# Kernel tuning notes

Hardware: AMD Instinct MI355X
Metric: run time of the kernel (lower is better)

Reference implementation:

```python
import jax, jax.numpy as jnp
import numpy as np

D_MODEL = 2048
N_LATENTS = 64
D_LATENT = 1024
N_HEADS = 16
D_H = D_LATENT // N_HEADS


def _split_heads(t):
    B, T, _ = t.shape
    return t.reshape(B, T, N_HEADS, D_H).transpose(0, 2, 1, 3)  # [B,H,T,d_h]


def _merge_heads(t):
    B, H, T, d = t.shape
    return t.transpose(0, 2, 1, 3).reshape(B, T, H * d)


def _attn(Q, K, V):
    scores = jnp.einsum('bhqd,bhkd->bhqk', Q, K) / jnp.sqrt(jnp.asarray(D_H, Q.dtype))
    w = jax.nn.softmax(scores, axis=-1)
    return jnp.einsum('bhqk,bhkd->bhqd', w, V)


def setup_inputs() -> dict:
    key = jax.random.key(0)
    ks = jax.random.split(key, 9)
    s_in = 1.0 / np.sqrt(D_MODEL)
    s_lat = 1.0 / np.sqrt(D_LATENT)
    return {
        'x': jax.random.normal(ks[0], (4, 4096, D_MODEL), dtype=jnp.float32),
        'L': jax.random.normal(ks[1], (N_LATENTS, D_LATENT), dtype=jnp.float32),
        'W_q_lat': jax.random.normal(ks[2], (D_LATENT, D_LATENT), dtype=jnp.float32) * s_lat,
        'W_k_in': jax.random.normal(ks[3], (D_MODEL, D_LATENT), dtype=jnp.float32) * s_in,
        'W_v_in': jax.random.normal(ks[4], (D_MODEL, D_LATENT), dtype=jnp.float32) * s_in,
        'W_q_in': jax.random.normal(ks[5], (D_MODEL, D_LATENT), dtype=jnp.float32) * s_in,
        'W_k_lat': jax.random.normal(ks[6], (D_LATENT, D_LATENT), dtype=jnp.float32) * s_lat,
        'W_v_lat': jax.random.normal(ks[7], (D_LATENT, D_LATENT), dtype=jnp.float32) * s_lat,
        'W_out': jax.random.normal(ks[8], (D_LATENT, D_MODEL), dtype=jnp.float32) * s_lat,
    }


def reference(x, L, W_q_lat, W_k_in, W_v_in, W_q_in, W_k_lat, W_v_lat, W_out):
    B = x.shape[0]
    Lb = jnp.broadcast_to(L[None], (B, N_LATENTS, D_LATENT))
    # Stage 1: latents attend to input tokens (cross-attention)
    Q = _split_heads(Lb @ W_q_lat)
    K = _split_heads(x @ W_k_in)
    V = _split_heads(x @ W_v_in)
    z = _merge_heads(_attn(Q, K, V))  # [B, n_latents, d_latent]
    # Stage 2: latent self-attention
    Ql = _split_heads(z @ W_q_lat)
    Kl = _split_heads(z @ W_k_lat)
    Vl = _split_heads(z @ W_v_lat)
    z2 = _merge_heads(_attn(Ql, Kl, Vl))
    # Stage 3: input tokens attend to latents (cross-attention back)
    Qx = _split_heads(x @ W_q_in)
    Kz = _split_heads(z2 @ W_k_lat)
    Vz = _split_heads(z2 @ W_v_lat)
    x_latent = _merge_heads(_attn(Qx, Kz, Vz))  # [B, N, d_latent]
    return x_latent @ W_out
```

## Files before the change

kernel.cpp:

```cpp
#include <hip/hip_runtime.h>


#define SEQ      4096
#define NHEADS   16
#define SCALE    0.125f

typedef short bfrag __attribute__((ext_vector_type(8)));
typedef float facc  __attribute__((ext_vector_type(4)));

__device__ __forceinline__ unsigned short f2bf(float f) {
  unsigned u = __float_as_uint(f);
  u += 0x7FFFu + ((u >> 16) & 1u);
  return (unsigned short)(u >> 16);
}
__device__ __forceinline__ float bf2f(unsigned short h) {
  return __uint_as_float(((unsigned)h) << 16);
}
__device__ __forceinline__ unsigned pack_hl(float a, float b, unsigned &lo) {
  unsigned short ha = f2bf(a), hb = f2bf(b);
  unsigned short la = f2bf(a - bf2f(ha)), lb = f2bf(b - bf2f(hb));
  lo = (unsigned)la | ((unsigned)lb << 16);
  return (unsigned)ha | ((unsigned)hb << 16);
}

__device__ __forceinline__ void gl_lds16(const void* g, void* l) {
  __builtin_amdgcn_global_load_lds(
      (const __attribute__((address_space(1))) void*)g,
      (__attribute__((address_space(3))) void*)l, 16, 0, 0);
}

__device__ __forceinline__ void write_split16(unsigned short* Hp, unsigned short* Lp,
                                              const float* o, float inv) {
  uint4 H0, H1, L0, L1;
  unsigned* Hw = &H0.x; unsigned* Lw = &L0.x;
#pragma unroll
  for (int k = 0; k < 8; k++) {
    unsigned lo;
    unsigned hi = pack_hl(o[2*k] * inv, o[2*k+1] * inv, lo);
    if (k < 4) { (&H0.x)[k] = hi; (&L0.x)[k] = lo; }
    else       { (&H1.x)[k-4] = hi; (&L1.x)[k-4] = lo; }
  }
  (void)Hw; (void)Lw;
  *(uint4*)Hp       = H0;
  *(uint4*)(Hp + 8) = H1;
  *(uint4*)Lp       = L0;
  *(uint4*)(Lp + 8) = L1;
}

__global__ __launch_bounds__(256) void prep_weight_kernel(
    const float* __restrict__ W, int K, int N,
    unsigned short* __restrict__ Th, unsigned short* __restrict__ Tl)
{
  __shared__ float tile[64][68];
  const int k0 = blockIdx.x * 64, n0 = blockIdx.y * 64;
  const int tid = threadIdx.x;
  const int r = tid >> 2, q = tid & 3;
#pragma unroll
  for (int j = 0; j < 4; j++)
    *(float4*)&tile[r][q*16 + j*4] =
        *(const float4*)&W[(size_t)(k0 + r) * N + n0 + q*16 + j*4];
  __syncthreads();
  const size_t obase = (size_t)(n0 + r) * K + k0 + q*16;
#pragma unroll
  for (int g = 0; g < 2; g++) {
    float f[8];
#pragma unroll
    for (int e = 0; e < 8; e++) f[e] = tile[q*16 + g*8 + e][r];
    uint4 H, Lo;
    H.x = pack_hl(f[0], f[1], Lo.x);
    H.y = pack_hl(f[2], f[3], Lo.y);
    H.z = pack_hl(f[4], f[5], Lo.z);
    H.w = pack_hl(f[6], f[7], Lo.w);
    *(uint4*)&Th[obase + g*8] = H;
    *(uint4*)&Tl[obase + g*8] = Lo;
  }
}

__global__ __launch_bounds__(256) void split_f32_kernel(
    const float* __restrict__ X, unsigned short* __restrict__ H,
    unsigned short* __restrict__ Lo, int n8)
{
  int idx = blockIdx.x * 256 + threadIdx.x;
  if (idx >= n8) return;
  const float4 a = *(const float4*)&X[(size_t)idx*8];
  const float4 b = *(const float4*)&X[(size_t)idx*8 + 4];
  uint4 Hh, Ll;
  Hh.x = pack_hl(a.x, a.y, Ll.x);
  Hh.y = pack_hl(a.z, a.w, Ll.y);
  Hh.z = pack_hl(b.x, b.y, Ll.z);
  Hh.w = pack_hl(b.z, b.w, Ll.w);
  *(uint4*)&H[(size_t)idx*8]  = Hh;
  *(uint4*)&Lo[(size_t)idx*8] = Ll;
}

__global__ __launch_bounds__(256, 2) void gemm_dma_kernel(
    const unsigned short* __restrict__ Ah, const unsigned short* __restrict__ Al,
    const unsigned short* __restrict__ Bh, const unsigned short* __restrict__ Bl,
    float* __restrict__ C, int M, int N, int K)
{
  __shared__ unsigned short sAh[256*32], sAl[256*32], sBh[128*32], sBl[128*32];
  const int tid = threadIdx.x;
  const int m0 = blockIdx.x * 256, n0 = blockIdx.y * 128;
  const int wave = tid >> 6, lane = tid & 63;
  const int lrow = lane & 15, lq = lane >> 4;
  const int wm = (wave & 1) * 128, wn = (wave >> 1) * 64;

  const int srow = lane >> 2, schunk = lane & 3;
  size_t aoff[4], boff[2];
#pragma unroll
  for (int j = 0; j < 4; j++) {
    int rg = m0 + 64*wave + 16*j + srow;
    if (rg > M-1) rg = M-1;
    aoff[j] = ((size_t)rg * K + schunk*8) * 2;
  }
#pragma unroll
  for (int j = 0; j < 2; j++) {
    int rg = n0 + 32*wave + 16*j + srow;
    boff[j] = ((size_t)rg * K + schunk*8) * 2;
  }
  const char* Ahc = (const char*)Ah;  const char* Alc = (const char*)Al;
  const char* Bhc = (const char*)Bh;  const char* Blc = (const char*)Bl;

  facc acc[8][4] = {};

  for (int k0 = 0; k0 < K; k0 += 32) {
    const size_t kb = (size_t)k0 * 2;
#pragma unroll
    for (int j = 0; j < 4; j++) {
      gl_lds16(Ahc + aoff[j] + kb, (char*)sAh + (64*wave + 16*j)*64);
      gl_lds16(Alc + aoff[j] + kb, (char*)sAl + (64*wave + 16*j)*64);
    }
#pragma unroll
    for (int j = 0; j < 2; j++) {
      gl_lds16(Bhc + boff[j] + kb, (char*)sBh + (32*wave + 16*j)*64);
      gl_lds16(Blc + boff[j] + kb, (char*)sBl + (32*wave + 16*j)*64);
    }
    __syncthreads();

    bfrag bh[4], bl[4];
#pragma unroll
    for (int ni = 0; ni < 4; ni++) {
      const int bo = (wn + ni*16 + lrow)*32 + lq*8;
      bh[ni] = *(const bfrag*)&sBh[bo];
      bl[ni] = *(const bfrag*)&sBl[bo];
    }
#pragma unroll
    for (int mi = 0; mi < 8; mi++) {
      const int ao = (wm + mi*16 + lrow)*32 + lq*8;
      const bfrag ah = *(const bfrag*)&sAh[ao];
      const bfrag al = *(const bfrag*)&sAl[ao];
#pragma unroll
      for (int ni = 0; ni < 4; ni++) {
        acc[mi][ni] = __builtin_amdgcn_mfma_f32_16x16x32_bf16(ah, bh[ni], acc[mi][ni], 0, 0, 0);
        acc[mi][ni] = __builtin_amdgcn_mfma_f32_16x16x32_bf16(ah, bl[ni], acc[mi][ni], 0, 0, 0);
        acc[mi][ni] = __builtin_amdgcn_mfma_f32_16x16x32_bf16(al, bh[ni], acc[mi][ni], 0, 0, 0);
      }
    }
    __syncthreads();
  }

#pragma unroll
  for (int mi = 0; mi < 8; mi++) {
#pragma unroll
    for (int r = 0; r < 4; r++) {
      const int row = m0 + wm + mi*16 + lq*4 + r;
      if (row < M) {
        float* Crow = C + (size_t)row * N + n0 + wn + lrow;
#pragma unroll
        for (int ni = 0; ni < 4; ni++)
          Crow[ni*16] = acc[mi][ni][r];
      }
    }
  }
}

__global__ __launch_bounds__(256) void attn1_kernel(
    const float* __restrict__ Qlat,
    const float* __restrict__ KV,
    float* __restrict__ mPart, float* __restrict__ lPart, float* __restrict__ oPart)
{
  __shared__ float Ks[64][68], Vs[64][68], Ps[64][68];
  const int tid = threadIdx.x;
  const int chunk = blockIdx.x, h = blockIdx.y, b = blockIdx.z;
  const int i = tid >> 2, q = tid & 3, db = q * 16, rot = q * 20;

  float4 qreg[16];
#pragma unroll
  for (int dd = 0; dd < 16; dd++) {
    const int c = (4*dd + rot) & 63;
    qreg[dd] = *(const float4*)&Qlat[(size_t)i*1024 + h*64 + c];
  }
  float m_i = -__builtin_inff(), l_i = 0.f;
  float o[16];
#pragma unroll
  for (int dd = 0; dd < 16; dd++) o[dd] = 0.f;

  for (int kt = 0; kt < 8; kt++) {
    const int jg = chunk*512 + kt*64;
    const size_t rb = ((size_t)b*SEQ + jg + i) * 2048;
#pragma unroll
    for (int jj = 0; jj < 4; jj++) {
      *(float4*)&Ks[i][db + jj*4] = *(const float4*)&KV[rb + h*64 + db + jj*4];
      *(float4*)&Vs[i][db + jj*4] = *(const float4*)&KV[rb + 1024 + h*64 + db + jj*4];
    }
    __syncthreads();

    float s[16];
#pragma unroll
    for (int jj = 0; jj < 16; jj++) {
      const int j = db + jj;
      float4 a4 = make_float4(0.f, 0.f, 0.f, 0.f);
#pragma unroll
      for (int dd = 0; dd < 16; dd++) {
        const int c = (4*dd + rot) & 63;
        const float4 kv = *(const float4*)&Ks[j][c];
        a4.x += qreg[dd].x*kv.x; a4.y += qreg[dd].y*kv.y;
        a4.z += qreg[dd].z*kv.z; a4.w += qreg[dd].w*kv.w;
      }
      s[jj] = (a4.x + a4.y + a4.z + a4.w) * SCALE;
    }
    float mt = s[0];
#pragma unroll
    for (int jj = 1; jj < 16; jj++) mt = fmaxf(mt, s[jj]);
    mt = fmaxf(mt, __shfl_xor(mt, 1));
    mt = fmaxf(mt, __shfl_xor(mt, 2));
    const float m_new = fmaxf(m_i, mt);
    const float fac = __expf(m_i - m_new);
    l_i *= fac;
#pragma unroll
    for (int dd = 0; dd < 16; dd++) o[dd] *= fac;
    float ps = 0.f;
#pragma unroll
    for (int jj = 0; jj < 16; jj++) {
      const float p = __expf(s[jj] - m_new);
      Ps[i][db + jj] = p;
      ps += p;
    }
    ps += __shfl_xor(ps, 1);
    ps += __shfl_xor(ps, 2);
    l_i += ps;
    m_i = m_new;
    __syncthreads();
    for (int j = 0; j < 64; j++) {
      const float w = Ps[i][j];
#pragma unroll
      for (int dd = 0; dd < 16; dd += 4) {
        const float4 vv = *(const float4*)&Vs[j][db + dd];
        o[dd+0] += w*vv.x; o[dd+1] += w*vv.y; o[dd+2] += w*vv.z; o[dd+3] += w*vv.w;
      }
    }
    __syncthreads();
  }
  const int bh = b*NHEADS + h;
  const size_t ob = ((size_t)(bh*8 + chunk)*64 + i)*64 + db;
#pragma unroll
  for (int dd = 0; dd < 16; dd++) oPart[ob + dd] = o[dd];
  if (q == 0) {
    mPart[(bh*8 + chunk)*64 + i] = m_i;
    lPart[(bh*8 + chunk)*64 + i] = l_i;
  }
}

__global__ __launch_bounds__(256) void attn1_combine_kernel(
    const float* __restrict__ mPart, const float* __restrict__ lPart,
    const float* __restrict__ oPart,
    unsigned short* __restrict__ Zh, unsigned short* __restrict__ Zl)
{
  const int h = blockIdx.x, b = blockIdx.y;
  const int tid = threadIdx.x;
  const int i = tid >> 2, q = tid & 3, db = q * 16;
  const int bh = b*NHEADS + h;
  float mv[8];
  float M = -__builtin_inff();
#pragma unroll
  for (int c = 0; c < 8; c++) { mv[c] = mPart[(bh*8 + c)*64 + i]; M = fmaxf(M, mv[c]); }
  float Lt = 0.f, w[8];
#pragma unroll
  for (int c = 0; c < 8; c++) { w[c] = __expf(mv[c] - M); Lt += lPart[(bh*8 + c)*64 + i] * w[c]; }
  float o[16];
#pragma unroll
  for (int dd = 0; dd < 16; dd++) o[dd] = 0.f;
#pragma unroll
  for (int c = 0; c < 8; c++) {
    const float* ob = oPart + ((size_t)(bh*8 + c)*64 + i)*64 + db;
#pragma unroll
    for (int dd = 0; dd < 16; dd += 4) {
      const float4 v = *(const float4*)(ob + dd);
      o[dd+0] += w[c]*v.x; o[dd+1] += w[c]*v.y; o[dd+2] += w[c]*v.z; o[dd+3] += w[c]*v.w;
    }
  }
  const float inv = 1.f / Lt;
  const size_t ob2 = ((size_t)b*64 + i)*1024 + h*64 + db;
  write_split16(Zh + ob2, Zl + ob2, o, inv);
}

__global__ __launch_bounds__(256) void attn_small_kernel(
    const float* __restrict__ Qp, int ldq, int qrows_per_b,
    const float* __restrict__ Kp, int ldk,
    const float* __restrict__ Vp, int ldv,
    unsigned short* __restrict__ Oh, unsigned short* __restrict__ Ol, int ldo)
{
  __shared__ float Ks[64][68], Vs[64][68], Ps[64][68];
  const int tid = threadIdx.x;
  const int tt = blockIdx.x, h = blockIdx.y, b = blockIdx.z;
  const int i = tid >> 2, q = tid & 3, db = q * 16, rot = q * 20;
  const size_t qrow = (size_t)b*qrows_per_b + (size_t)tt*64 + i;
  const size_t krow = (size_t)b*64 + i;

  float4 qreg[16];
#pragma unroll
  for (int dd = 0; dd < 16; dd++) {
    const int c = (4*dd + rot) & 63;
    qreg[dd] = *(const float4*)&Qp[qrow*ldq + h*64 + c];
  }
#pragma unroll
  for (int jj = 0; jj < 4; jj++) {
    *(float4*)&Ks[i][db + jj*4] = *(const float4*)&Kp[krow*ldk + h*64 + db + jj*4];
    *(float4*)&Vs[i][db + jj*4] = *(const float4*)&Vp[krow*ldv + h*64 + db + jj*4];
  }
  __syncthreads();

  float s[16];
#pragma unroll
  for (int jj = 0; jj < 16; jj++) {
    const int j = db + jj;
    float4 a4 = make_float4(0.f, 0.f, 0.f, 0.f);
#pragma unroll
    for (int dd = 0; dd < 16; dd++) {
      const int c = (4*dd + rot) & 63;
      const float4 kv = *(const float4*)&Ks[j][c];
      a4.x += qreg[dd].x*kv.x; a4.y += qreg[dd].y*kv.y;
      a4.z += qreg[dd].z*kv.z; a4.w += qreg[dd].w*kv.w;
    }
    s[jj] = (a4.x + a4.y + a4.z + a4.w) * SCALE;
  }
  float m = s[0];
#pragma unroll
  for (int jj = 1; jj < 16; jj++) m = fmaxf(m, s[jj]);
  m = fmaxf(m, __shfl_xor(m, 1));
  m = fmaxf(m, __shfl_xor(m, 2));
  float l = 0.f;
#pragma unroll
  for (int jj = 0; jj < 16; jj++) {
    const float p = __expf(s[jj] - m);
    Ps[i][db + jj] = p;
    l += p;
  }
  l += __shfl_xor(l, 1);
  l += __shfl_xor(l, 2);
  __syncthreads();
  float o[16];
#pragma unroll
  for (int dd = 0; dd < 16; dd++) o[dd] = 0.f;
  for (int j = 0; j < 64; j++) {
    const float w = Ps[i][j];
#pragma unroll
    for (int dd = 0; dd < 16; dd += 4) {
      const float4 vv = *(const float4*)&Vs[j][db + dd];
      o[dd+0] += w*vv.x; o[dd+1] += w*vv.y; o[dd+2] += w*vv.z; o[dd+3] += w*vv.w;
    }
  }
  const float inv = 1.f / l;
  const size_t ob = qrow*ldo + h*64 + db;
  write_split16(Oh + ob, Ol + ob, o, inv);
}

extern "C" void kernel_launch(void* const* d_in, const int* in_sizes, int n_in,
                              void* d_out, int out_size, void* d_ws, size_t ws_size,
                              hipStream_t stream)
{
  const float* x      = (const float*)d_in[0];
  const float* L      = (const float*)d_in[1];
  const float* Wq_lat = (const float*)d_in[2];
  const float* Wk_in  = (const float*)d_in[3];
  const float* Wv_in  = (const float*)d_in[4];
  const float* Wq_in  = (const float*)d_in[5];
  const float* Wk_lat = (const float*)d_in[6];
  const float* Wv_lat = (const float*)d_in[7];
  const float* Wout   = (const float*)d_in[8];
  float* out = (float*)d_out;
  (void)in_sizes; (void)n_in; (void)out_size; (void)ws_size;

  char* ws = (char*)d_ws;
  size_t off = 0;
  auto alloc = [&](size_t bytes) -> char* {
    char* p = ws + off; off += (bytes + 255) & ~(size_t)255; return p;
  };
  unsigned short* wtKV_h  = (unsigned short*)alloc(2048ull*2048*2);
  unsigned short* wtKV_l  = (unsigned short*)alloc(2048ull*2048*2);
  unsigned short* wtQin_h = (unsigned short*)alloc(1024ull*2048*2);
  unsigned short* wtQin_l = (unsigned short*)alloc(1024ull*2048*2);
  unsigned short* wtLat_h = (unsigned short*)alloc(3072ull*1024*2);
  unsigned short* wtLat_l = (unsigned short*)alloc(3072ull*1024*2);
  unsigned short* wtOut_h = (unsigned short*)alloc(2048ull*1024*2);
  unsigned short* wtOut_l = (unsigned short*)alloc(2048ull*1024*2);
  unsigned short* xh    = (unsigned short*)alloc(16384ull*2048*2);
  unsigned short* xl    = (unsigned short*)alloc(16384ull*2048*2);
  unsigned short* Lh    = (unsigned short*)alloc(64ull*1024*2);
  unsigned short* Ll    = (unsigned short*)alloc(64ull*1024*2);
  unsigned short* zh    = (unsigned short*)alloc(256ull*1024*2);
  unsigned short* zl    = (unsigned short*)alloc(256ull*1024*2);
  unsigned short* z2h   = (unsigned short*)alloc(256ull*1024*2);
  unsigned short* z2l   = (unsigned short*)alloc(256ull*1024*2);
  float* qlat  = (float*)alloc(64ull*1024*4);
  float* zqkv  = (float*)alloc(256ull*3072*4);
  float* z2kv  = (float*)alloc(256ull*2048*4);
  float* mPart = (float*)alloc(4ull*16*8*64*4);
  float* lPart = (float*)alloc(4ull*16*8*64*4);
  float* oPart = (float*)alloc(4ull*16*8*64*64*4);
  float* big   = (float*)alloc(16384ull*2048*4);
  float* qx    = big;
  unsigned short* xlat_h = (unsigned short*)(big + 16384ull*1024);
  unsigned short* xlat_l = xlat_h + 16384ull*1024;

  dim3 blk(256);

  prep_weight_kernel<<<dim3(32, 16), blk, 0, stream>>>(Wk_in, 2048, 1024, wtKV_h, wtKV_l);
  prep_weight_kernel<<<dim3(32, 16), blk, 0, stream>>>(Wv_in, 2048, 1024, wtKV_h + 1024ull*2048, wtKV_l + 1024ull*2048);
  prep_weight_kernel<<<dim3(32, 16), blk, 0, stream>>>(Wq_in, 2048, 1024, wtQin_h, wtQin_l);
  prep_weight_kernel<<<dim3(16, 16), blk, 0, stream>>>(Wq_lat, 1024, 1024, wtLat_h, wtLat_l);
  prep_weight_kernel<<<dim3(16, 16), blk, 0, stream>>>(Wk_lat, 1024, 1024, wtLat_h + 1024ull*1024, wtLat_l + 1024ull*1024);
  prep_weight_kernel<<<dim3(16, 16), blk, 0, stream>>>(Wv_lat, 1024, 1024, wtLat_h + 2048ull*1024, wtLat_l + 2048ull*1024);
  prep_weight_kernel<<<dim3(16, 32), blk, 0, stream>>>(Wout, 1024, 2048, wtOut_h, wtOut_l);
  split_f32_kernel<<<dim3(16384), blk, 0, stream>>>(x, xh, xl, 16384*2048/8);
  split_f32_kernel<<<dim3(32), blk, 0, stream>>>(L, Lh, Ll, 64*1024/8);

  gemm_dma_kernel<<<dim3(1, 8), blk, 0, stream>>>(Lh, Ll, wtLat_h, wtLat_l, qlat, 64, 1024, 1024);
  gemm_dma_kernel<<<dim3(64, 16), blk, 0, stream>>>(xh, xl, wtKV_h, wtKV_l, big, 16384, 2048, 2048);
  attn1_kernel<<<dim3(8, 16, 4), blk, 0, stream>>>(qlat, big, mPart, lPart, oPart);
  attn1_combine_kernel<<<dim3(16, 4), blk, 0, stream>>>(mPart, lPart, oPart, zh, zl);
  gemm_dma_kernel<<<dim3(1, 24), blk, 0, stream>>>(zh, zl, wtLat_h, wtLat_l, zqkv, 256, 3072, 1024);
  attn_small_kernel<<<dim3(1, 16, 4), blk, 0, stream>>>(zqkv, 3072, 64, zqkv + 1024, 3072, zqkv + 2048, 3072, z2h, z2l, 1024);
  gemm_dma_kernel<<<dim3(1, 16), blk, 0, stream>>>(z2h, z2l, wtLat_h + 1024ull*1024, wtLat_l + 1024ull*1024, z2kv, 256, 2048, 1024);
  gemm_dma_kernel<<<dim3(64, 8), blk, 0, stream>>>(xh, xl, wtQin_h, wtQin_l, qx, 16384, 1024, 2048);
  attn_small_kernel<<<dim3(64, 16, 4), blk, 0, stream>>>(qx, 1024, 4096, z2kv, 2048, z2kv + 1024, 2048, xlat_h, xlat_l, 1024);
  gemm_dma_kernel<<<dim3(64, 16), blk, 0, stream>>>(xlat_h, xlat_l, wtOut_h, wtOut_l, out, 16384, 2048, 1024);
}
```

Before: 1.348 ms.

## Fuse Q projection into KV GEMM, swizzle LDS, add MFMA stage-3 attention

Concatenates W_q_in with W_k_in/W_v_in so one GEMM produces K, V and Qx together, and reuses the x hi/lo buffers for the stage-3 output. Adds an XOR-style rotation of 16-byte chunks in the GEMM's LDS staging to reduce bank conflicts on fragment reads. Replaces the scalar FP32 stage-3 attention with an MFMA kernel that splits Q, K and V into bf16 hi/lo pairs. P is rounded to a single bf16, so accuracy drops slightly in exchange for matrix-core throughput.

Result: faster. 1.282 ms (-4.9%).

```diff
diff --git a/kernel.cpp b/kernel.cpp
--- a/kernel.cpp
+++ b/kernel.cpp
@@ -22,6 +22,14 @@
   lo = (unsigned)la | ((unsigned)lb << 16);
   return (unsigned)ha | ((unsigned)hb << 16);
 }
+__device__ __forceinline__ void split8(const float* f, bfrag &h, bfrag &l) {
+#pragma unroll
+  for (int j = 0; j < 8; j++) {
+    unsigned short hi = f2bf(f[j]);
+    h[j] = (short)hi;
+    l[j] = (short)f2bf(f[j] - bf2f(hi));
+  }
+}
 
 __device__ __forceinline__ void gl_lds16(const void* g, void* l) {
   __builtin_amdgcn_global_load_lds(
@@ -32,7 +40,6 @@
 __device__ __forceinline__ void write_split16(unsigned short* Hp, unsigned short* Lp,
                                               const float* o, float inv) {
   uint4 H0, H1, L0, L1;
-  unsigned* Hw = &H0.x; unsigned* Lw = &L0.x;
 #pragma unroll
   for (int k = 0; k < 8; k++) {
     unsigned lo;
@@ -40,7 +47,6 @@
     if (k < 4) { (&H0.x)[k] = hi; (&L0.x)[k] = lo; }
     else       { (&H1.x)[k-4] = hi; (&L1.x)[k-4] = lo; }
   }
-  (void)Hw; (void)Lw;
   *(uint4*)Hp       = H0;
   *(uint4*)(Hp + 8) = H1;
   *(uint4*)Lp       = L0;
@@ -109,14 +115,18 @@
   size_t aoff[4], boff[2];
 #pragma unroll
   for (int j = 0; j < 4; j++) {
-    int rg = m0 + 64*wave + 16*j + srow;
+    const int R = 64*wave + 16*j + srow;
+    int rg = m0 + R;
     if (rg > M-1) rg = M-1;
-    aoff[j] = ((size_t)rg * K + schunk*8) * 2;
+    const int c = (schunk - (R >> 1)) & 3;
+    aoff[j] = ((size_t)rg * K + c*8) * 2;
   }
 #pragma unroll
   for (int j = 0; j < 2; j++) {
-    int rg = n0 + 32*wave + 16*j + srow;
-    boff[j] = ((size_t)rg * K + schunk*8) * 2;
+    const int R = 32*wave + 16*j + srow;
+    const int rg = n0 + R;
+    const int c = (schunk - (R >> 1)) & 3;
+    boff[j] = ((size_t)rg * K + c*8) * 2;
   }
   const char* Ahc = (const char*)Ah;  const char* Alc = (const char*)Al;
   const char* Bhc = (const char*)Bh;  const char* Blc = (const char*)Bl;
@@ -140,13 +150,17 @@
     bfrag bh[4], bl[4];
 #pragma unroll
     for (int ni = 0; ni < 4; ni++) {
-      const int bo = (wn + ni*16 + lrow)*32 + lq*8;
+      const int R = wn + ni*16 + lrow;
+      const int slot = (lq + (R >> 1)) & 3;
+      const int bo = R*32 + slot*8;
       bh[ni] = *(const bfrag*)&sBh[bo];
       bl[ni] = *(const bfrag*)&sBl[bo];
     }
 #pragma unroll
     for (int mi = 0; mi < 8; mi++) {
-      const int ao = (wm + mi*16 + lrow)*32 + lq*8;
+      const int R = wm + mi*16 + lrow;
+      const int slot = (lq + (R >> 1)) & 3;
+      const int ao = R*32 + slot*8;
       const bfrag ah = *(const bfrag*)&sAh[ao];
       const bfrag al = *(const bfrag*)&sAl[ao];
 #pragma unroll
@@ -197,7 +211,7 @@
 
   for (int kt = 0; kt < 8; kt++) {
     const int jg = chunk*512 + kt*64;
-    const size_t rb = ((size_t)b*SEQ + jg + i) * 2048;
+    const size_t rb = ((size_t)b*SEQ + jg + i) * 3072;
 #pragma unroll
     for (int jj = 0; jj < 4; jj++) {
       *(float4*)&Ks[i][db + jj*4] = *(const float4*)&KV[rb + h*64 + db + jj*4];
@@ -363,6 +377,110 @@
   const float inv = 1.f / l;
   const size_t ob = qrow*ldo + h*64 + db;
   write_split16(Oh + ob, Ol + ob, o, inv);
+}
+
+__global__ __launch_bounds__(256) void attn3_mfma_kernel(
+    const float* __restrict__ QKV,
+    const float* __restrict__ z2kv,
+    unsigned short* __restrict__ Oh, unsigned short* __restrict__ Ol)
+{
+  __shared__ unsigned short Pb[4][16][72];
+  const int tid = threadIdx.x;
+  const int wave = tid >> 6, lane = tid & 63;
+  const int lrow = lane & 15, lq = lane >> 4;
+  const int qt = blockIdx.x, h = blockIdx.y, b = blockIdx.z;
+  const size_t tok0 = (size_t)b*SEQ + qt*64 + wave*16;
+
+  bfrag qh[2], ql[2];
+  {
+    const float* qp = QKV + (tok0 + lrow)*3072 + 2048 + h*64 + lq*8;
+#pragma unroll
+    for (int ks = 0; ks < 2; ks++) {
+      float f[8];
+      *(float4*)&f[0] = *(const float4*)(qp + ks*32);
+      *(float4*)&f[4] = *(const float4*)(qp + ks*32 + 4);
+      split8(f, qh[ks], ql[ks]);
+    }
+  }
+  bfrag kh[4][2], kl[4][2];
+#pragma unroll
+  for (int ni = 0; ni < 4; ni++) {
+    const float* kp = z2kv + (size_t)(b*64 + ni*16 + lrow)*2048 + h*64 + lq*8;
+#pragma unroll
+    for (int ks = 0; ks < 2; ks++) {
+      float f[8];
+      *(float4*)&f[0] = *(const float4*)(kp + ks*32);
+      *(float4*)&f[4] = *(const float4*)(kp + ks*32 + 4);
+      split8(f, kh[ni][ks], kl[ni][ks]);
+    }
+  }
+  facc s[4] = {};
+#pragma unroll
+  for (int ni = 0; ni < 4; ni++)
+#pragma unroll
+    for (int ks = 0; ks < 2; ks++) {
+      s[ni] = __builtin_amdgcn_mfma_f32_16x16x32_bf16(qh[ks], kh[ni][ks], s[ni], 0, 0, 0);
+      s[ni] = __builtin_amdgcn_mfma_f32_16x16x32_bf16(qh[ks], kl[ni][ks], s[ni], 0, 0, 0);
+      s[ni] = __builtin_amdgcn_mfma_f32_16x16x32_bf16(ql[ks], kh[ni][ks], s[ni], 0, 0, 0);
+    }
+  float inv[4];
+  float p[4][4];
+#pragma unroll
+  for (int r = 0; r < 4; r++) {
+    float mx = fmaxf(fmaxf(s[0][r], s[1][r]), fmaxf(s[2][r], s[3][r])) * SCALE;
+    mx = fmaxf(mx, __shfl_xor(mx, 1));
+    mx = fmaxf(mx, __shfl_xor(mx, 2));
+    mx = fmaxf(mx, __shfl_xor(mx, 4));
+    mx = fmaxf(mx, __shfl_xor(mx, 8));
+    float sum = 0.f;
+#pragma unroll
+    for (int ni = 0; ni < 4; ni++) {
+      p[ni][r] = __expf(s[ni][r] * SCALE - mx);
+      sum += p[ni][r];
+    }
+    sum += __shfl_xor(sum, 1);
+    sum += __shfl_xor(sum, 2);
+    sum += __shfl_xor(sum, 4);
+    sum += __shfl_xor(sum, 8);
+    inv[r] = 1.f / sum;
+  }
+#pragma unroll
+  for (int ni = 0; ni < 4; ni++)
+#pragma unroll
+    for (int r = 0; r < 4; r++)
+      Pb[wave][lq*4 + r][ni*16 + lrow] = f2bf(p[ni][r]);
+  __asm__ volatile("s_waitcnt lgkmcnt(0)" ::: "memory");
+  bfrag pa[2];
+#pragma unroll
+  for (int ks = 0; ks < 2; ks++)
+    pa[ks] = *(const bfrag*)&Pb[wave][lrow][ks*32 + lq*8];
+  facc o[4] = {};
+#pragma unroll
+  for (int ni = 0; ni < 4; ni++) {
+#pragma unroll
+    for (int ks = 0; ks < 2; ks++) {
+      float f[8];
+#pragma unroll
+      for (int jj = 0; jj < 8; jj++)
+        f[jj] = z2kv[(size_t)(b*64 + ks*32 + lq*8 + jj)*2048 + 1024 + h*64 + ni*16 + lrow];
+      bfrag vh, vl;
+      split8(f, vh, vl);
+      o[ni] = __builtin_amdgcn_mfma_f32_16x16x32_bf16(pa[ks], vh, o[ni], 0, 0, 0);
+      o[ni] = __builtin_amdgcn_mfma_f32_16x16x32_bf16(pa[ks], vl, o[ni], 0, 0, 0);
+    }
+  }
+#pragma unroll
+  for (int ni = 0; ni < 4; ni++) {
+#pragma unroll
+    for (int r = 0; r < 4; r++) {
+      const float v = o[ni][r] * inv[r];
+      const unsigned short hi = f2bf(v);
+      const unsigned short lo = f2bf(v - bf2f(hi));
+      const size_t idx = (tok0 + lq*4 + r)*1024 + h*64 + ni*16 + lrow;
+      Oh[idx] = hi;
+      Ol[idx] = lo;
+    }
+  }
 }
 
 extern "C" void kernel_launch(void* const* d_in, const int* in_sizes, int n_in,
@@ -386,10 +504,8 @@
   auto alloc = [&](size_t bytes) -> char* {
     char* p = ws + off; off += (bytes + 255) & ~(size_t)255; return p;
   };
-  unsigned short* wtKV_h  = (unsigned short*)alloc(2048ull*2048*2);
-  unsigned short* wtKV_l  = (unsigned short*)alloc(2048ull*2048*2);
-  unsigned short* wtQin_h = (unsigned short*)alloc(1024ull*2048*2);
-  unsigned short* wtQin_l = (unsigned short*)alloc(1024ull*2048*2);
+  unsigned short* wtKVQ_h = (unsigned short*)alloc(3072ull*2048*2);
+  unsigned short* wtKVQ_l = (unsigned short*)alloc(3072ull*2048*2);
   unsigned short* wtLat_h = (unsigned short*)alloc(3072ull*1024*2);
   unsigned short* wtLat_l = (unsigned short*)alloc(3072ull*1024*2);
   unsigned short* wtOut_h = (unsigned short*)alloc(2048ull*1024*2);
@@ -408,16 +524,15 @@
   float* mPart = (float*)alloc(4ull*16*8*64*4);
   float* lPart = (float*)alloc(4ull*16*8*64*4);
   float* oPart = (float*)alloc(4ull*16*8*64*64*4);
-  float* big   = (float*)alloc(16384ull*2048*4);
-  float* qx    = big;
-  unsigned short* xlat_h = (unsigned short*)(big + 16384ull*1024);
-  unsigned short* xlat_l = xlat_h + 16384ull*1024;
+  float* qkv   = (float*)alloc(16384ull*3072*4);
+  unsigned short* xlat_h = xh;
+  unsigned short* xlat_l = xl;
 
   dim3 blk(256);
 
-  prep_weight_kernel<<<dim3(32, 16), blk, 0, stream>>>(Wk_in, 2048, 1024, wtKV_h, wtKV_l);
-  prep_weight_kernel<<<dim3(32, 16), blk, 0, stream>>>(Wv_in, 2048, 1024, wtKV_h + 1024ull*2048, wtKV_l + 1024ull*2048);
-  prep_weight_kernel<<<dim3(32, 16), blk, 0, stream>>>(Wq_in, 2048, 1024, wtQin_h, wtQin_l);
+  prep_weight_kernel<<<dim3(32, 16), blk, 0, stream>>>(Wk_in, 2048, 1024, wtKVQ_h, wtKVQ_l);
+  prep_weight_kernel<<<dim3(32, 16), blk, 0, stream>>>(Wv_in, 2048, 1024, wtKVQ_h + 1024ull*2048, wtKVQ_l + 1024ull*2048);
+  prep_weight_kernel<<<dim3(32, 16), blk, 0, stream>>>(Wq_in, 2048, 1024, wtKVQ_h + 2048ull*2048, wtKVQ_l + 2048ull*2048);
   prep_weight_kernel<<<dim3(16, 16), blk, 0, stream>>>(Wq_lat, 1024, 1024, wtLat_h, wtLat_l);
   prep_weight_kernel<<<dim3(16, 16), blk, 0, stream>>>(Wk_lat, 1024, 1024, wtLat_h + 1024ull*1024, wtLat_l + 1024ull*1024);
   prep_weight_kernel<<<dim3(16, 16), blk, 0, stream>>>(Wv_lat, 1024, 1024, wtLat_h + 2048ull*1024, wtLat_l + 2048ull*1024);
@@ -426,13 +541,12 @@
   split_f32_kernel<<<dim3(32), blk, 0, stream>>>(L, Lh, Ll, 64*1024/8);
 
   gemm_dma_kernel<<<dim3(1, 8), blk, 0, stream>>>(Lh, Ll, wtLat_h, wtLat_l, qlat, 64, 1024, 1024);
-  gemm_dma_kernel<<<dim3(64, 16), blk, 0, stream>>>(xh, xl, wtKV_h, wtKV_l, big, 16384, 2048, 2048);
-  attn1_kernel<<<dim3(8, 16, 4), blk, 0, stream>>>(qlat, big, mPart, lPart, oPart);
+  gemm_dma_kernel<<<dim3(64, 24), blk, 0, stream>>>(xh, xl, wtKVQ_h, wtKVQ_l, qkv, 16384, 3072, 2048);
+  attn1_kernel<<<dim3(8, 16, 4), blk, 0, stream>>>(qlat, qkv, mPart, lPart, oPart);
   attn1_combine_kernel<<<dim3(16, 4), blk, 0, stream>>>(mPart, lPart, oPart, zh, zl);
   gemm_dma_kernel<<<dim3(1, 24), blk, 0, stream>>>(zh, zl, wtLat_h, wtLat_l, zqkv, 256, 3072, 1024);
   attn_small_kernel<<<dim3(1, 16, 4), blk, 0, stream>>>(zqkv, 3072, 64, zqkv + 1024, 3072, zqkv + 2048, 3072, z2h, z2l, 1024);
   gemm_dma_kernel<<<dim3(1, 16), blk, 0, stream>>>(z2h, z2l, wtLat_h + 1024ull*1024, wtLat_l + 1024ull*1024, z2kv, 256, 2048, 1024);
-  gemm_dma_kernel<<<dim3(64, 8), blk, 0, stream>>>(xh, xl, wtQin_h, wtQin_l, qx, 16384, 1024, 2048);
-  attn_small_kernel<<<dim3(64, 16, 4), blk, 0, stream>>>(qx, 1024, 4096, z2kv, 2048, z2kv + 1024, 2048, xlat_h, xlat_l, 1024);
+  attn3_mfma_kernel<<<dim3(64, 16, 4), blk, 0, stream>>>(qkv, z2kv, xlat_h, xlat_l);
   gemm_dma_kernel<<<dim3(64, 16), blk, 0, stream>>>(xlat_h, xlat_l, wtOut_h, wtOut_l, out, 16384, 2048, 1024);
 }
```
